# Kernel optimization log

Hardware: AMD Instinct MI355X
Metric: run time of the kernel (lower is better)

The kernel has to match this reference:

```python
import jax, jax.numpy as jnp
import numpy as np

N_HEADS = 8
NEG_INF = -1e30  # finite stand-in for -inf in masked_fill (exact 0 prob after softmax)


def apply_rotary_emb(x, cos, sin):
    # x: [B, H, T, hd]; cos/sin: [T, hd] -> broadcast over B, H
    d = x.shape[-1]
    x1, x2 = x[..., : d // 2], x[..., d // 2 :]
    x_rot = jnp.concatenate((-x2, x1), axis=-1)
    return x * cos[None, None] + x_rot * sin[None, None]


def setup_inputs() -> dict:
    key = jax.random.key(0)
    ks = jax.random.split(key, 5)
    B, T, C, hd = 4, 2048, 512, 64
    x = jax.random.normal(ks[0], (B, T, C), dtype=jnp.float32)
    cos = jax.random.uniform(ks[1], (T, hd), dtype=jnp.float32)
    sin = jax.random.uniform(ks[2], (T, hd), dtype=jnp.float32)
    # xavier_uniform-ish scale for linear weights
    W_qkv = jax.random.normal(ks[3], (3 * C, C), dtype=jnp.float32) * (1.0 / np.sqrt(C))
    W_out = jax.random.normal(ks[4], (C, C), dtype=jnp.float32) * (1.0 / np.sqrt(C))
    return {"x": x, "cos": cos, "sin": sin, "W_qkv": W_qkv, "W_out": W_out}


def reference(x, cos, sin, W_qkv, W_out):
    B, T, C = x.shape
    H = N_HEADS
    hd = C // H
    # qkv projection (torch Linear: y = x @ W^T), split into q, k, v as [B, H, T, hd]
    qkv = (x @ W_qkv.T).reshape(B, T, 3, H, hd)
    qkv = jnp.transpose(qkv, (2, 0, 3, 1, 4))
    q, k, v = qkv[0], qkv[1], qkv[2]
    # RoPE on q, k
    q = apply_rotary_emb(q, cos[:T], sin[:T])
    k = apply_rotary_emb(k, cos[:T], sin[:T])
    scale = jnp.sqrt(jnp.float32(hd))
    attn = jnp.einsum("bhqd,bhkd->bhqk", q, k) / scale  # [B, H, T, T]
    causal = jnp.tril(jnp.ones((T, T), dtype=bool))
    attn = jnp.where(causal[None, None], attn, NEG_INF)
    attn = jax.nn.softmax(attn, axis=-1)
    out = jnp.einsum("bhqk,bhkd->bhqd", attn, v)  # [B, H, T, hd]
    out = jnp.transpose(out, (0, 2, 1, 3)).reshape(B, T, C)
    return out @ W_out.T
```

## Files before the change

### kernel.cpp

```cpp
#include <hip/hip_runtime.h>
#include <hip/hip_bf16.h>

#define B_SZ 4
#define T_SZ 2048
#define C_SZ 512
#define H_SZ 8
#define HD 64
#define QSCALE 0.1803368801111137f

typedef __bf16 bf16;
typedef __bf16 bf16x8 __attribute__((ext_vector_type(8)));
typedef float f32x4 __attribute__((ext_vector_type(4)));

__device__ __forceinline__ f32x4 mfma16(bf16x8 a, bf16x8 b, f32x4 c) {
    return __builtin_amdgcn_mfma_f32_16x16x32_bf16(a, b, c, 0, 0, 0);
}

#define GLD_LDS16(g, l) __builtin_amdgcn_global_load_lds( \
    (__attribute__((address_space(1))) void*)(void*)(g),  \
    (__attribute__((address_space(3))) void*)(l), 16, 0, 0)

__global__ __launch_bounds__(256) void cvt_all(
    const float* __restrict__ x, const float* __restrict__ wqkv,
    const float* __restrict__ wout, bf16* __restrict__ xb,
    bf16* __restrict__ wqb, bf16* __restrict__ wob) {
  int i = blockIdx.x * 256 + threadIdx.x;
  const int n0 = (B_SZ*T_SZ*C_SZ)/4, n1 = (3*C_SZ*C_SZ)/4, n2 = (C_SZ*C_SZ)/4;
  const float4* s; bf16* d; int j;
  if (i < n0)                { s = (const float4*)x;    d = xb;  j = i; }
  else if (i < n0 + n1)      { s = (const float4*)wqkv; d = wqb; j = i - n0; }
  else if (i < n0 + n1 + n2) { s = (const float4*)wout; d = wob; j = i - n0 - n1; }
  else return;
  float4 v = s[j];
  union { bf16 h[4]; uint2 u; } p;
  p.h[0] = (bf16)v.x; p.h[1] = (bf16)v.y; p.h[2] = (bf16)v.z; p.h[3] = (bf16)v.w;
  *(uint2*)(d + (size_t)j * 4) = p.u;
}

template<int EPI>
__global__ __launch_bounds__(256) void gemm_bt(
    const bf16* __restrict__ A, const bf16* __restrict__ Bw,
    int M, int N, int K,
    void* __restrict__ o0, void* __restrict__ o1, void* __restrict__ o2) {
  __shared__ bf16 sA[128 * 32];
  __shared__ bf16 sB[128 * 32];
  const int tid = threadIdx.x;
  const int m0 = blockIdx.x * 128, n0 = blockIdx.y * 128;
  const int w = tid >> 6, lane = tid & 63, quad = lane >> 4, l16 = lane & 15;
  const int wm = (w >> 1) * 64, wn = (w & 1) * 64;
  const int srow = tid >> 2, scol = (tid & 3) * 8;
  f32x4 acc[4][4] = {};
  for (int k0 = 0; k0 < K; k0 += 32) {
    __syncthreads();
    const bf16* ga = A  + (size_t)(m0 + srow) * K + k0 + scol;
    const bf16* gb = Bw + (size_t)(n0 + srow) * K + k0 + scol;
    GLD_LDS16(ga,                 sA + tid * 8);
    GLD_LDS16(ga + (size_t)64*K,  sA + tid * 8 + 2048);
    GLD_LDS16(gb,                 sB + tid * 8);
    GLD_LDS16(gb + (size_t)64*K,  sB + tid * 8 + 2048);
    __syncthreads();
    bf16x8 af[4], bfr[4];
#pragma unroll
    for (int i = 0; i < 4; i++)
      af[i] = *(const bf16x8*)(sA + (wm + i*16 + l16) * 32 + quad * 8);
#pragma unroll
    for (int j = 0; j < 4; j++)
      bfr[j] = *(const bf16x8*)(sB + (wn + j*16 + l16) * 32 + quad * 8);
#pragma unroll
    for (int i = 0; i < 4; i++)
#pragma unroll
      for (int j = 0; j < 4; j++)
        acc[i][j] = mfma16(af[i], bfr[j], acc[i][j]);
  }
  if (EPI == 0) {
    const int three = n0 >> 9;
    bf16* dst = three == 0 ? (bf16*)o0 : (three == 1 ? (bf16*)o1 : (bf16*)o2);
#pragma unroll
    for (int i = 0; i < 4; i++) {
#pragma unroll
      for (int j = 0; j < 4; j++) {
        const int n = n0 + wn + j*16 + l16;
        const int h = (n & 511) >> 6, dcol = n & 63;
#pragma unroll
        for (int r = 0; r < 4; r++) {
          const int m = m0 + wm + i*16 + quad*4 + r;
          const int b = m >> 11, t = m & (T_SZ - 1);
          if (three < 2)
            dst[(((size_t)(b*H_SZ + h)) * T_SZ + t) * HD + dcol] = (bf16)acc[i][j][r];
          else
            dst[(((size_t)(b*H_SZ + h)) * HD + dcol) * T_SZ + t] = (bf16)acc[i][j][r];
        }
      }
    }
  } else {
    float* dst = (float*)o0;
#pragma unroll
    for (int i = 0; i < 4; i++)
#pragma unroll
      for (int j = 0; j < 4; j++)
#pragma unroll
        for (int r = 0; r < 4; r++) {
          const int m = m0 + wm + i*16 + quad*4 + r;
          const int n = n0 + wn + j*16 + l16;
          dst[(size_t)m * N + n] = acc[i][j][r];
        }
  }
}

__global__ __launch_bounds__(256) void rope_qk(
    bf16* __restrict__ q, bf16* __restrict__ k,
    const float* __restrict__ cp, const float* __restrict__ sp) {
  const int i = blockIdx.x * 256 + threadIdx.x;
  const int d  = i & 31;
  const int t  = (i >> 5) & (T_SZ - 1);
  const int bh = i >> 16;
  const size_t base = ((size_t)bh * T_SZ + t) * HD;
  const float c1 = cp[t*HD + d], c2 = cp[t*HD + d + 32];
  const float s1 = sp[t*HD + d], s2 = sp[t*HD + d + 32];
  float a = (float)q[base + d], b = (float)q[base + d + 32];
  q[base + d]      = (bf16)((a * c1 - b * s1) * QSCALE);
  q[base + d + 32] = (bf16)((b * c2 + a * s2) * QSCALE);
  a = (float)k[base + d]; b = (float)k[base + d + 32];
  k[base + d]      = (bf16)(a * c1 - b * s1);
  k[base + d + 32] = (bf16)(b * c2 + a * s2);
}

__global__ __launch_bounds__(256) void flash_attn(
    const bf16* __restrict__ qb, const bf16* __restrict__ kb,
    const bf16* __restrict__ vtb, bf16* __restrict__ ao) {
  __shared__ bf16 sK[2][64 * 64];
  __shared__ bf16 sVT[2][64 * 64];
  __shared__ bf16 sP[4][2560];
  const int tid = threadIdx.x, w = tid >> 6, lane = tid & 63;
  const int quad = lane >> 4, l16 = lane & 15;
  const int bh = blockIdx.x & 31;
  const int qi = 15 - (blockIdx.x >> 5);
  const int q0w = qi * 128 + w * 32;
  const bf16* Q  = qb  + (size_t)bh * T_SZ * HD;
  const bf16* Kp = kb  + (size_t)bh * T_SZ * HD;
  const bf16* Vt = vtb + (size_t)bh * HD * T_SZ;
  bf16x8 qf[2][2];
#pragma unroll
  for (int nt = 0; nt < 2; nt++)
#pragma unroll
    for (int ds = 0; ds < 2; ds++)
      qf[nt][ds] = *(const bf16x8*)(Q + (size_t)(q0w + nt*16 + l16) * HD + ds*32 + quad*8);
  float l_[2] = {0.f, 0.f};
  f32x4 ot[4][2] = {};
  bf16* sPw = &sP[w][0];
  const int srow = tid >> 3, scg = (tid & 7) ^ (srow & 7);
  const int ntiles = (qi + 1) * 2;
  GLD_LDS16(Kp + (size_t)srow * HD + scg*8,          sK[0]  + tid*8);
  GLD_LDS16(Kp + (size_t)(srow + 32) * HD + scg*8,   sK[0]  + tid*8 + 2048);
  GLD_LDS16(Vt + (size_t)srow * T_SZ + scg*8,        sVT[0] + tid*8);
  GLD_LDS16(Vt + (size_t)(srow + 32) * T_SZ + scg*8, sVT[0] + tid*8 + 2048);
  for (int it = 0; it < ntiles; it++) {
    const int kt = it * 64;
    __syncthreads();
    if (it + 1 < ntiles) {
      const int kn = kt + 64;
      bf16* dK = sK[(it + 1) & 1];
      bf16* dV = sVT[(it + 1) & 1];
      GLD_LDS16(Kp + (size_t)(kn + srow) * HD + scg*8,        dK + tid*8);
      GLD_LDS16(Kp + (size_t)(kn + srow + 32) * HD + scg*8,   dK + tid*8 + 2048);
      GLD_LDS16(Vt + (size_t)srow * T_SZ + kn + scg*8,        dV + tid*8);
      GLD_LDS16(Vt + (size_t)(srow + 32) * T_SZ + kn + scg*8, dV + tid*8 + 2048);
    }
    if (kt > q0w + 31) continue;
    const bf16* cK = sK[it & 1];
    const bf16* cV = sVT[it & 1];
    f32x4 st[4][2] = {};
#pragma unroll
    for (int mt = 0; mt < 4; mt++) {
#pragma unroll
      for (int ds = 0; ds < 2; ds++) {
        const int row = mt*16 + l16, cl = ds*4 + quad;
        const bf16x8 kf = *(const bf16x8*)(cK + row*64 + (cl ^ (row & 7)) * 8);
#pragma unroll
        for (int nt = 0; nt < 2; nt++)
          st[mt][nt] = mfma16(kf, qf[nt][ds], st[mt][nt]);
      }
    }
    if (kt + 63 > q0w) {
#pragma unroll
      for (int nt = 0; nt < 2; nt++) {
        const int qg = q0w + nt*16 + l16;
        const int kb0 = kt + quad*4;
#pragma unroll
        for (int mt = 0; mt < 4; mt++)
#pragma unroll
          for (int r = 0; r < 4; r++)
            st[mt][nt][r] = (kb0 + mt*16 + r <= qg) ? st[mt][nt][r] : -1e30f;
      }
    }
#pragma unroll
    for (int nt = 0; nt < 2; nt++) {
      float sum = 0.f;
#pragma unroll
      for (int mt = 0; mt < 4; mt++) {
        union { bf16 h[4]; unsigned long long ull; } pk;
#pragma unroll
        for (int r = 0; r < 4; r++) {
          const float p = __builtin_amdgcn_exp2f(st[mt][nt][r]);
          sum += p;
          pk.h[r] = (bf16)p;
        }
        *(unsigned long long*)(sPw + (mt>>1)*1280 + (nt*16 + l16)*40 + (mt&1)*16 + quad*4) = pk.ull;
      }
      l_[nt] += sum;
    }
    asm volatile("" ::: "memory");
    bf16x8 pf[2][2];
#pragma unroll
    for (int nt = 0; nt < 2; nt++)
#pragma unroll
      for (int s = 0; s < 2; s++)
        pf[nt][s] = *(const bf16x8*)(sPw + s*1280 + (nt*16 + l16)*40 + quad*8);
#pragma unroll
    for (int dt = 0; dt < 4; dt++) {
#pragma unroll
      for (int s = 0; s < 2; s++) {
        const int row = dt*16 + l16, cl = s*4 + quad;
        const bf16x8 vf = *(const bf16x8*)(cV + row*64 + (cl ^ (row & 7)) * 8);
#pragma unroll
        for (int nt = 0; nt < 2; nt++)
          ot[dt][nt] = mfma16(vf, pf[nt][s], ot[dt][nt]);
      }
    }
  }
  float lt[2];
#pragma unroll
  for (int nt = 0; nt < 2; nt++) {
    float s = l_[nt];
    s += __shfl_xor(s, 16);
    s += __shfl_xor(s, 32);
    lt[nt] = 1.f / s;
  }
#pragma unroll
  for (int dt = 0; dt < 4; dt++)
#pragma unroll
    for (int nt = 0; nt < 2; nt++) {
      union { bf16 h[4]; unsigned long long ull; } pk;
#pragma unroll
      for (int r = 0; r < 4; r++) pk.h[r] = (bf16)(ot[dt][nt][r] * lt[nt]);
      *(unsigned long long*)(sPw + (nt*16 + l16)*72 + dt*16 + quad*4) = pk.ull;
    }
  asm volatile("" ::: "memory");
  const int oq = lane >> 1, half = lane & 1;
  const int b = bh >> 3, h = bh & 7;
  const int tg = qi*128 + w*32 + oq;
  bf16* dst = ao + ((size_t)(b * T_SZ + tg)) * C_SZ + h * HD + half * 32;
#pragma unroll
  for (int j = 0; j < 4; j++)
    *(uint4*)(dst + j*8) = *(const uint4*)(sPw + oq*72 + half*32 + j*8);
}

extern "C" void kernel_launch(void* const* d_in, const int* in_sizes, int n_in,
                              void* d_out, int out_size, void* d_ws, size_t ws_size,
                              hipStream_t stream) {
  const float* x    = (const float*)d_in[0];
  const float* cosp = (const float*)d_in[1];
  const float* sinp = (const float*)d_in[2];
  const float* wqkv = (const float*)d_in[3];
  const float* wout = (const float*)d_in[4];
  char* ws = (char*)d_ws;
  bf16* xb    = (bf16*)(ws);
  bf16* wqkvb = (bf16*)(ws +  8388608);
  bf16* woutb = (bf16*)(ws +  9961472);
  bf16* qbuf  = (bf16*)(ws + 10485760);
  bf16* kbuf  = (bf16*)(ws + 18874368);
  bf16* vtbuf = (bf16*)(ws + 27262976);
  bf16* ao    = (bf16*)(ws + 35651584);

  cvt_all<<<dim3(5120), dim3(256), 0, stream>>>(x, wqkv, wout, xb, wqkvb, woutb);
  gemm_bt<0><<<dim3(64, 12), dim3(256), 0, stream>>>(
      xb, wqkvb, B_SZ * T_SZ, 3 * C_SZ, C_SZ,
      (void*)qbuf, (void*)kbuf, (void*)vtbuf);
  rope_qk<<<dim3(8192), dim3(256), 0, stream>>>(qbuf, kbuf, cosp, sinp);
  flash_attn<<<dim3(512), dim3(256), 0, stream>>>(qbuf, kbuf, vtbuf, ao);
  gemm_bt<1><<<dim3(64, 4), dim3(256), 0, stream>>>(
      ao, woutb, B_SZ * T_SZ, C_SZ, C_SZ,
      (void*)d_out, nullptr, nullptr);
}
```

Baseline: 173.9 us.

## Pair causal query tiles per block to balance flash attention work

Each flash attention block now handles two query tiles, qi=15-pj and qi=pj, so every block walks the same total of 34 key tiles. The grid is halved to 256 blocks. The goal is to remove the load imbalance of causal attention, where late query tiles did far more work than early ones. In exchange, each block runs serially over both tiles, and there are fewer blocks than the 256 CUs can hold in parallel, so occupancy and latency hiding may drop.

```diff
diff --git a/kernel.cpp b/kernel.cpp
--- a/kernel.cpp
+++ b/kernel.cpp
@@ -134,8 +134,11 @@
   const int tid = threadIdx.x, w = tid >> 6, lane = tid & 63;
   const int quad = lane >> 4, l16 = lane & 15;
   const int bh = blockIdx.x & 31;
-  const int qi = 15 - (blockIdx.x >> 5);
-  const int q0w = qi * 128 + w * 32;
+  const int pj = blockIdx.x >> 5;
+  const int nA = (16 - pj) * 2;
+  const int ntot = 34;
+  int qi = 15 - pj;
+  int q0w = qi * 128 + w * 32;
   const bf16* Q  = qb  + (size_t)bh * T_SZ * HD;
   const bf16* Kp = kb  + (size_t)bh * T_SZ * HD;
   const bf16* Vt = vtb + (size_t)bh * HD * T_SZ;
@@ -149,16 +152,46 @@
   f32x4 ot[4][2] = {};
   bf16* sPw = &sP[w][0];
   const int srow = tid >> 3, scg = (tid & 7) ^ (srow & 7);
-  const int ntiles = (qi + 1) * 2;
+  const int b = bh >> 3, h = bh & 7;
+
+  auto epilogue = [&]() {
+    float lt[2];
+#pragma unroll
+    for (int nt = 0; nt < 2; nt++) {
+      float s = l_[nt];
+      s += __shfl_xor(s, 16);
+      s += __shfl_xor(s, 32);
+      lt[nt] = 1.f / s;
+    }
+#pragma unroll
+    for (int dt = 0; dt < 4; dt++)
+#pragma unroll
+      for (int nt = 0; nt < 2; nt++) {
+        union { bf16 h4[4]; unsigned long long ull; } pk;
+#pragma unroll
+        for (int r = 0; r < 4; r++) pk.h4[r] = (bf16)(ot[dt][nt][r] * lt[nt]);
+        *(unsigned long long*)(sPw + (nt*16 + l16)*72 + dt*16 + quad*4) = pk.ull;
+      }
+    asm volatile("" ::: "memory");
+    const int oq = lane >> 1, half = lane & 1;
+    const int tg = qi*128 + w*32 + oq;
+    bf16* dst = ao + ((size_t)(b * T_SZ + tg)) * C_SZ + h * HD + half * 32;
+#pragma unroll
+    for (int j = 0; j < 4; j++)
+      *(uint4*)(dst + j*8) = *(const uint4*)(sPw + oq*72 + half*32 + j*8);
+    asm volatile("" ::: "memory");
+  };
+
   GLD_LDS16(Kp + (size_t)srow * HD + scg*8,          sK[0]  + tid*8);
   GLD_LDS16(Kp + (size_t)(srow + 32) * HD + scg*8,   sK[0]  + tid*8 + 2048);
   GLD_LDS16(Vt + (size_t)srow * T_SZ + scg*8,        sVT[0] + tid*8);
   GLD_LDS16(Vt + (size_t)(srow + 32) * T_SZ + scg*8, sVT[0] + tid*8 + 2048);
-  for (int it = 0; it < ntiles; it++) {
-    const int kt = it * 64;
+
+  for (int it = 0; it < ntot; it++) {
+    const int kt = (it < nA ? it : it - nA) * 64;
     __syncthreads();
-    if (it + 1 < ntiles) {
-      const int kn = kt + 64;
+    if (it + 1 < ntot) {
+      const int kn = (it + 1 < nA ? it + 1 : it + 1 - nA) * 64;
       bf16* dK = sK[(it + 1) & 1];
       bf16* dV = sVT[(it + 1) & 1];
       GLD_LDS16(Kp + (size_t)(kn + srow) * HD + scg*8,        dK + tid*8);
@@ -166,93 +199,85 @@
       GLD_LDS16(Vt + (size_t)srow * T_SZ + kn + scg*8,        dV + tid*8);
       GLD_LDS16(Vt + (size_t)(srow + 32) * T_SZ + kn + scg*8, dV + tid*8 + 2048);
     }
-    if (kt > q0w + 31) continue;
-    const bf16* cK = sK[it & 1];
-    const bf16* cV = sVT[it & 1];
-    f32x4 st[4][2] = {};
-#pragma unroll
-    for (int mt = 0; mt < 4; mt++) {
-#pragma unroll
-      for (int ds = 0; ds < 2; ds++) {
-        const int row = mt*16 + l16, cl = ds*4 + quad;
-        const bf16x8 kf = *(const bf16x8*)(cK + row*64 + (cl ^ (row & 7)) * 8);
+    if (kt <= q0w + 31) {
+      const bf16* cK = sK[it & 1];
+      const bf16* cV = sVT[it & 1];
+      f32x4 st[4][2] = {};
+#pragma unroll
+      for (int mt = 0; mt < 4; mt++) {
+#pragma unroll
+        for (int ds = 0; ds < 2; ds++) {
+          const int row = mt*16 + l16, cl = ds*4 + quad;
+          const bf16x8 kf = *(const bf16x8*)(cK + row*64 + (cl ^ (row & 7)) * 8);
+#pragma unroll
+          for (int nt = 0; nt < 2; nt++)
+            st[mt][nt] = mfma16(kf, qf[nt][ds], st[mt][nt]);
+        }
+      }
+      if (kt + 63 > q0w) {
+#pragma unroll
+        for (int nt = 0; nt < 2; nt++) {
+          const int qg = q0w + nt*16 + l16;
+          const int kb0 = kt + quad*4;
+#pragma unroll
+          for (int mt = 0; mt < 4; mt++)
+#pragma unroll
+            for (int r = 0; r < 4; r++)
+              st[mt][nt][r] = (kb0 + mt*16 + r <= qg) ? st[mt][nt][r] : -1e30f;
+        }
+      }
+#pragma unroll
+      for (int nt = 0; nt < 2; nt++) {
+        float sum = 0.f;
+#pragma unroll
+        for (int mt = 0; mt < 4; mt++) {
+          union { bf16 h4[4]; unsigned long long ull; } pk;
+#pragma unroll
+          for (int r = 0; r < 4; r++) {
+            const float p = __builtin_amdgcn_exp2f(st[mt][nt][r]);
+            sum += p;
+            pk.h4[r] = (bf16)p;
+          }
+          *(unsigned long long*)(sPw + (mt>>1)*1280 + (nt*16 + l16)*40 + (mt&1)*16 + quad*4) = pk.ull;
+        }
+        l_[nt] += sum;
+      }
+      asm volatile("" ::: "memory");
+      bf16x8 pf[2][2];
+#pragma unroll
+      for (int nt = 0; nt < 2; nt++)
+#pragma unroll
+        for (int s = 0; s < 2; s++)
+          pf[nt][s] = *(const bf16x8*)(sPw + s*1280 + (nt*16 + l16)*40 + quad*8);
+#pragma unroll
+      for (int dt = 0; dt < 4; dt++) {
+#pragma unroll
+        for (int s = 0; s < 2; s++) {
+          const int row = dt*16 + l16, cl = s*4 + quad;
+          const bf16x8 vf = *(const bf16x8*)(cV + row*64 + (cl ^ (row & 7)) * 8);
+#pragma unroll
+          for (int nt = 0; nt < 2; nt++)
+            ot[dt][nt] = mfma16(vf, pf[nt][s], ot[dt][nt]);
+        }
+      }
+    }
+    if (it == nA - 1) {
+      epilogue();
+      qi = pj; q0w = qi * 128 + w * 32;
+#pragma unroll
+      for (int nt = 0; nt < 2; nt++)
+#pragma unroll
+        for (int ds = 0; ds < 2; ds++)
+          qf[nt][ds] = *(const bf16x8*)(Q + (size_t)(q0w + nt*16 + l16) * HD + ds*32 + quad*8);
+      l_[0] = 0.f; l_[1] = 0.f;
+#pragma unroll
+      for (int dt = 0; dt < 4; dt++)
 #pragma unroll
         for (int nt = 0; nt < 2; nt++)
-          st[mt][nt] = mfma16(kf, qf[nt][ds], st[mt][nt]);
-      }
-    }
-    if (kt + 63 > q0w) {
-#pragma unroll
-      for (int nt = 0; nt < 2; nt++) {
-        const int qg = q0w + nt*16 + l16;
-        const int kb0 = kt + quad*4;
-#pragma unroll
-        for (int mt = 0; mt < 4; mt++)
-#pragma unroll
-          for (int r = 0; r < 4; r++)
-            st[mt][nt][r] = (kb0 + mt*16 + r <= qg) ? st[mt][nt][r] : -1e30f;
-      }
-    }
-#pragma unroll
-    for (int nt = 0; nt < 2; nt++) {
-      float sum = 0.f;
-#pragma unroll
-      for (int mt = 0; mt < 4; mt++) {
-        union { bf16 h[4]; unsigned long long ull; } pk;
-#pragma unroll
-        for (int r = 0; r < 4; r++) {
-          const float p = __builtin_amdgcn_exp2f(st[mt][nt][r]);
-          sum += p;
-          pk.h[r] = (bf16)p;
-        }
-        *(unsigned long long*)(sPw + (mt>>1)*1280 + (nt*16 + l16)*40 + (mt&1)*16 + quad*4) = pk.ull;
-      }
-      l_[nt] += sum;
-    }
-    asm volatile("" ::: "memory");
-    bf16x8 pf[2][2];
-#pragma unroll
-    for (int nt = 0; nt < 2; nt++)
-#pragma unroll
-      for (int s = 0; s < 2; s++)
-        pf[nt][s] = *(const bf16x8*)(sPw + s*1280 + (nt*16 + l16)*40 + quad*8);
-#pragma unroll
-    for (int dt = 0; dt < 4; dt++) {
-#pragma unroll
-      for (int s = 0; s < 2; s++) {
-        const int row = dt*16 + l16, cl = s*4 + quad;
-        const bf16x8 vf = *(const bf16x8*)(cV + row*64 + (cl ^ (row & 7)) * 8);
-#pragma unroll
-        for (int nt = 0; nt < 2; nt++)
-          ot[dt][nt] = mfma16(vf, pf[nt][s], ot[dt][nt]);
-      }
+          ot[dt][nt] = f32x4{0.f, 0.f, 0.f, 0.f};
     }
   }
-  float lt[2];
-#pragma unroll
-  for (int nt = 0; nt < 2; nt++) {
-    float s = l_[nt];
-    s += __shfl_xor(s, 16);
-    s += __shfl_xor(s, 32);
-    lt[nt] = 1.f / s;
-  }
-#pragma unroll
-  for (int dt = 0; dt < 4; dt++)
-#pragma unroll
-    for (int nt = 0; nt < 2; nt++) {
-      union { bf16 h[4]; unsigned long long ull; } pk;
-#pragma unroll
-      for (int r = 0; r < 4; r++) pk.h[r] = (bf16)(ot[dt][nt][r] * lt[nt]);
-      *(unsigned long long*)(sPw + (nt*16 + l16)*72 + dt*16 + quad*4) = pk.ull;
-    }
-  asm volatile("" ::: "memory");
-  const int oq = lane >> 1, half = lane & 1;
-  const int b = bh >> 3, h = bh & 7;
-  const int tg = qi*128 + w*32 + oq;
-  bf16* dst = ao + ((size_t)(b * T_SZ + tg)) * C_SZ + h * HD + half * 32;
-#pragma unroll
-  for (int j = 0; j < 4; j++)
-    *(uint4*)(dst + j*8) = *(const uint4*)(sPw + oq*72 + half*32 + j*8);
+  epilogue();
 }
 
 extern "C" void kernel_launch(void* const* d_in, const int* in_sizes, int n_in,
@@ -277,7 +302,7 @@
       xb, wqkvb, B_SZ * T_SZ, 3 * C_SZ, C_SZ,
       (void*)qbuf, (void*)kbuf, (void*)vtbuf);
   rope_qk<<<dim3(8192), dim3(256), 0, stream>>>(qbuf, kbuf, cosp, sinp);
-  flash_attn<<<dim3(512), dim3(256), 0, stream>>>(qbuf, kbuf, vtbuf, ao);
+  flash_attn<<<dim3(256), dim3(256), 0, stream>>>(qbuf, kbuf, vtbuf, ao);
   gemm_bt<1><<<dim3(64, 4), dim3(256), 0, stream>>>(
       ao, woutb, B_SZ * T_SZ, C_SZ, C_SZ,
       (void*)d_out, nullptr, nullptr);
```

Result: no change. 177.0 us (+1.8%).
